# Kernel tuning notes

Hardware: AMD Instinct MI355X
Metric: run time of the kernel (lower is better)

## Reference

```python
import jax, jax.numpy as jnp
import numpy as np


def _mlp(x, w1, b1, w2, b2):
    # Linear -> Softplus -> Linear, matching nn.Sequential(Linear, Softplus, Linear)
    h = jax.nn.softplus(jnp.dot(x, w1.T) + b1)
    return jnp.dot(h, w2.T) + b2


def _forward(X, SC, w_init1, b_init1, w_init2, b_init2, w_eta1, b_eta1, w_eta2, b_eta2):
    N, L, _ = X.shape
    I = X[..., 1:2]   # [N, L, 1] current
    T = X[..., 2:3]   # [N, L, 1] temperature
    U = X[..., 3:4]   # [N, L, 1] voltage
    R = SC[..., 2:3]  # [N, 1]

    # SOC_init = SC[...,3:4] * (1 + SOC_init_net([I0, T0, U0, R]))
    init_feats = jnp.concatenate([I[:, 0], T[:, 0], U[:, 0], R], axis=-1)  # [N, 4]
    soc_init = SC[..., 3:4] * (1.0 + _mlp(init_feats, w_init1, b_init1, w_init2, b_init2))  # [N, 1]

    # delta_eta = eta_net([I, T])
    delta_eta = _mlp(jnp.concatenate([I, T], axis=-1), w_eta1, b_eta1, w_eta2, b_eta2)  # [N, L, 1]

    X_obs = jnp.concatenate([I, T, U, delta_eta], axis=-1)  # [N, L, 4]

    Q = SC[:, None, 0:1]      # [N, 1, 1]
    eta_0 = SC[:, None, 1:2]  # [N, 1, 1]
    # dy/dt does not depend on y -> Euler loop is an exact prefix sum.
    dy_dt = eta_0 * (1.0 + delta_eta) * I / (3600.0 * Q)  # [N, L, 1]

    # t_mask is all-True, so dt uses all 4 columns of X_obs (as in the source).
    dt = X_obs[:, 1:, :] - X_obs[:, :-1, :]        # [N, L-1, 4]
    inc = dt * dy_dt[:, :-1, :]                    # [N, L-1, 4]
    y_rest = soc_init[:, None, :] + jnp.cumsum(inc, axis=1)          # [N, L-1, 4]
    y0 = jnp.broadcast_to(soc_init[:, None, :], (N, 1, 4))           # [N, 1, 4]
    return jnp.concatenate([y0, y_rest], axis=1)   # [N, L, 4] == stack(dim=0).transpose(0,1)


def setup_inputs() -> dict:
    key = jax.random.key(0)
    ks = jax.random.split(key, 6)
    N, L = 4096, 4096
    X = jax.random.normal(ks[0], (N, L, 4), dtype=jnp.float32)
    # SC = [Q, eta_0, R, SOC_init_scale]; shift away from 0 so Q in denominator is safe
    SC = jax.random.uniform(ks[1], (N, 4), dtype=jnp.float32, minval=0.1, maxval=1.1)
    std = 0.1  # init_network_weights default
    return {
        "X": X,
        "SC": SC,
        "w_init1": std * jax.random.normal(ks[2], (1, 4), dtype=jnp.float32),
        "b_init1": jnp.zeros((1,), dtype=jnp.float32),
        "w_init2": std * jax.random.normal(ks[3], (1, 1), dtype=jnp.float32),
        "b_init2": jnp.zeros((1,), dtype=jnp.float32),
        "w_eta1": std * jax.random.normal(ks[4], (1, 2), dtype=jnp.float32),
        "b_eta1": jnp.zeros((1,), dtype=jnp.float32),
        "w_eta2": std * jax.random.normal(ks[5], (1, 1), dtype=jnp.float32),
        "b_eta2": jnp.zeros((1,), dtype=jnp.float32),
    }


def reference(X, SC, w_init1, b_init1, w_init2, b_init2, w_eta1, b_eta1, w_eta2, b_eta2):
    return _forward(X, SC, w_init1, b_init1, w_init2, b_init2,
                    w_eta1, b_eta1, w_eta2, b_eta2)
```

## Files before the change

### kernel.cpp

```cpp
#include <hip/hip_runtime.h>
#include <math.h>

#define BLOCK 256
#define NW (BLOCK / 64)

typedef float f32x4 __attribute__((ext_vector_type(4)));

__device__ __forceinline__ float sp(float x) {
    return fmaxf(x, 0.0f) + __logf(1.0f + __expf(-fabsf(x)));
}

__device__ __forceinline__ float wave_scan_f32(float s) {
    s += __int_as_float(__builtin_amdgcn_update_dpp(0, __float_as_int(s), 0x111, 0xf, 0xf, false));
    s += __int_as_float(__builtin_amdgcn_update_dpp(0, __float_as_int(s), 0x112, 0xf, 0xf, false));
    s += __int_as_float(__builtin_amdgcn_update_dpp(0, __float_as_int(s), 0x114, 0xf, 0xf, false));
    s += __int_as_float(__builtin_amdgcn_update_dpp(0, __float_as_int(s), 0x118, 0xf, 0xf, false));
    s += __int_as_float(__builtin_amdgcn_update_dpp(0, __float_as_int(s), 0x142, 0xa, 0xf, false));
    s += __int_as_float(__builtin_amdgcn_update_dpp(0, __float_as_int(s), 0x143, 0xc, 0xf, false));
    return s;
}

__device__ __forceinline__ void lds_barrier() {
    asm volatile("s_waitcnt lgkmcnt(0)\n\ts_barrier" ::: "memory");
}

__global__ __launch_bounds__(BLOCK) void socnet_kernel(
    const f32x4* __restrict__ X,
    const float*  __restrict__ SC,
    const float*  __restrict__ wi1, const float* __restrict__ bi1,
    const float*  __restrict__ wi2, const float* __restrict__ bi2,
    const float*  __restrict__ we1, const float* __restrict__ be1,
    const float*  __restrict__ we2, const float* __restrict__ be2,
    f32x4* __restrict__ Y, int L)
{
    const int n    = blockIdx.x;
    const int t    = threadIdx.x;
    const int wid  = t >> 6;

    const size_t rowoff = (size_t)n * (size_t)L;
    const f32x4* Xr = X + rowoff;
    f32x4*       Yr = Y + rowoff;

    const float W10 = we1[0], W11 = we1[1], B1 = be1[0];
    const float W2  = we2[0], B2e = be2[0];

    const float Q    = SC[n * 4 + 0];
    const float eta0 = SC[n * 4 + 1];
    const float R    = SC[n * 4 + 2];
    const float S3   = SC[n * 4 + 3];
    const float inv  = eta0 / (3600.0f * Q);

    const f32x4 x0 = Xr[0];
    const float h0 = sp(wi1[0] * x0.y + wi1[1] * x0.z + wi1[2] * x0.w + wi1[3] * R + bi1[0]);
    const float soc = S3 * (1.0f + (wi2[0] * h0 + bi2[0]));

    __shared__ f32x4 s_wsum[2][NW];

    f32x4 carry = (f32x4)(0.0f);

    const int ntiles = L / BLOCK;
    const int Lm1 = L - 1;

    int p = t;
    f32x4 xc0 = Xr[p];
    f32x4 xn0 = Xr[(p + 1 < L) ? (p + 1) : Lm1];
    f32x4 xc1 = Xr[(p + BLOCK < L) ? (p + BLOCK) : Lm1];
    f32x4 xn1 = Xr[(p + BLOCK + 1 < L) ? (p + BLOCK + 1) : Lm1];

    for (int tile = 0; tile < ntiles; ++tile) {
        const int pc = (p + 2 * BLOCK < L) ? (p + 2 * BLOCK) : Lm1;
        const int pn = (p + 2 * BLOCK + 1 < L) ? (p + 2 * BLOCK + 1) : Lm1;
        const f32x4 xc2 = Xr[pc];
        const f32x4 xn2 = Xr[pn];

        const float de_c = W2 * sp(W10 * xc0.y + W11 * xc0.z + B1) + B2e;
        const float de_n = W2 * sp(W10 * xn0.y + W11 * xn0.z + B1) + B2e;
        const float dy   = inv * (1.0f + de_c) * xc0.y;

        f32x4 inc;
        inc.x = (xn0.y - xc0.y) * dy;
        inc.y = (xn0.z - xc0.z) * dy;
        inc.z = (xn0.w - xc0.w) * dy;
        inc.w = (de_n - de_c) * dy;

        f32x4 scn;
        scn.x = wave_scan_f32(inc.x);
        scn.y = wave_scan_f32(inc.y);
        scn.z = wave_scan_f32(inc.z);
        scn.w = wave_scan_f32(inc.w);

        if ((t & 63) == 63) s_wsum[tile & 1][wid] = scn;
        lds_barrier();

        f32x4 excl = carry + scn - inc;
        #pragma unroll
        for (int w = 0; w < NW; ++w) {
            const f32x4 ws = s_wsum[tile & 1][w];
            if (w < wid) excl += ws;
            carry += ws;
        }

        const f32x4 yv = excl + (f32x4)(soc);
        __builtin_nontemporal_store(yv, &Yr[p]);

        xc0 = xc1; xn0 = xn1;
        xc1 = xc2; xn1 = xn2;
        p += BLOCK;
    }
}

extern "C" void kernel_launch(void* const* d_in, const int* in_sizes, int n_in,
                              void* d_out, int out_size, void* d_ws, size_t ws_size,
                              hipStream_t stream) {
    const f32x4* X   = (const f32x4*)d_in[0];
    const float* SC  = (const float*)d_in[1];
    const float* wi1 = (const float*)d_in[2];
    const float* bi1 = (const float*)d_in[3];
    const float* wi2 = (const float*)d_in[4];
    const float* bi2 = (const float*)d_in[5];
    const float* we1 = (const float*)d_in[6];
    const float* be1 = (const float*)d_in[7];
    const float* we2 = (const float*)d_in[8];
    const float* be2 = (const float*)d_in[9];
    f32x4* Y = (f32x4*)d_out;

    const int N = in_sizes[1] / 4;
    const int L = in_sizes[0] / (4 * N);

    socnet_kernel<<<N, BLOCK, 0, stream>>>(X, SC, wi1, bi1, wi2, bi2,
                                           we1, be1, we2, be2, Y, L);
}
```

Before: 93.54 us.

## Share neighbor observations via LDS instead of reloading shifted X rows

Each thread now loads only its own X element and computes its eta MLP value once, writing both to a double-buffered LDS array so the thread to its left can read them as its 'next' element. This removes the second shifted global load per element and the duplicate softplus evaluation. The prefetch depth goes from two tiles to three. The cost is extra LDS traffic, and the write into the next buffer relies on the existing per-tile barrier for ordering, which adds a dependency between tiles.

```diff
diff --git a/kernel.cpp b/kernel.cpp
--- a/kernel.cpp
+++ b/kernel.cpp
@@ -54,6 +54,7 @@
     const float h0 = sp(wi1[0] * x0.y + wi1[1] * x0.z + wi1[2] * x0.w + wi1[3] * R + bi1[0]);
     const float soc = S3 * (1.0f + (wi2[0] * h0 + bi2[0]));
 
+    __shared__ f32x4 s_obs[2][BLOCK + 1];
     __shared__ f32x4 s_wsum[2][NW];
 
     f32x4 carry = (f32x4)(0.0f);
@@ -63,25 +64,44 @@
 
     int p = t;
     f32x4 xc0 = Xr[p];
-    f32x4 xn0 = Xr[(p + 1 < L) ? (p + 1) : Lm1];
-    f32x4 xc1 = Xr[(p + BLOCK < L) ? (p + BLOCK) : Lm1];
-    f32x4 xn1 = Xr[(p + BLOCK + 1 < L) ? (p + BLOCK + 1) : Lm1];
+    f32x4 xc1 = Xr[(p + BLOCK     <= Lm1) ? p + BLOCK     : Lm1];
+    f32x4 xc2 = Xr[(p + 2 * BLOCK <= Lm1) ? p + 2 * BLOCK : Lm1];
+
+    float de0 = W2 * sp(W10 * xc0.y + W11 * xc0.z + B1) + B2e;
+    {
+        f32x4 ob; ob.x = xc0.y; ob.y = xc0.z; ob.z = xc0.w; ob.w = de0;
+        s_obs[0][t] = ob;
+        if (t == 0) {
+            const float d = W2 * sp(W10 * xc1.y + W11 * xc1.z + B1) + B2e;
+            f32x4 ob2; ob2.x = xc1.y; ob2.y = xc1.z; ob2.z = xc1.w; ob2.w = d;
+            s_obs[0][BLOCK] = ob2;
+        }
+    }
+    lds_barrier();
 
     for (int tile = 0; tile < ntiles; ++tile) {
-        const int pc = (p + 2 * BLOCK < L) ? (p + 2 * BLOCK) : Lm1;
-        const int pn = (p + 2 * BLOCK + 1 < L) ? (p + 2 * BLOCK + 1) : Lm1;
-        const f32x4 xc2 = Xr[pc];
-        const f32x4 xn2 = Xr[pn];
+        int ip = p + 3 * BLOCK; if (ip > Lm1) ip = Lm1;
+        const f32x4 xc3 = Xr[ip];
 
-        const float de_c = W2 * sp(W10 * xc0.y + W11 * xc0.z + B1) + B2e;
-        const float de_n = W2 * sp(W10 * xn0.y + W11 * xn0.z + B1) + B2e;
-        const float dy   = inv * (1.0f + de_c) * xc0.y;
+        const f32x4 nb = s_obs[tile & 1][t + 1];
 
+        const float de1 = W2 * sp(W10 * xc1.y + W11 * xc1.z + B1) + B2e;
+        {
+            f32x4 ob; ob.x = xc1.y; ob.y = xc1.z; ob.z = xc1.w; ob.w = de1;
+            s_obs[(tile + 1) & 1][t] = ob;
+            if (t == 0) {
+                const float d2 = W2 * sp(W10 * xc2.y + W11 * xc2.z + B1) + B2e;
+                f32x4 ob2; ob2.x = xc2.y; ob2.y = xc2.z; ob2.z = xc2.w; ob2.w = d2;
+                s_obs[(tile + 1) & 1][BLOCK] = ob2;
+            }
+        }
+
+        const float dy = inv * (1.0f + de0) * xc0.y;
         f32x4 inc;
-        inc.x = (xn0.y - xc0.y) * dy;
-        inc.y = (xn0.z - xc0.z) * dy;
-        inc.z = (xn0.w - xc0.w) * dy;
-        inc.w = (de_n - de_c) * dy;
+        inc.x = (nb.x - xc0.y) * dy;
+        inc.y = (nb.y - xc0.z) * dy;
+        inc.z = (nb.z - xc0.w) * dy;
+        inc.w = (nb.w - de0)  * dy;
 
         f32x4 scn;
         scn.x = wave_scan_f32(inc.x);
@@ -103,8 +123,9 @@
         const f32x4 yv = excl + (f32x4)(soc);
         __builtin_nontemporal_store(yv, &Yr[p]);
 
-        xc0 = xc1; xn0 = xn1;
-        xc1 = xc2; xn1 = xn2;
+        xc0 = xc1; de0 = de1;
+        xc1 = xc2;
+        xc2 = xc3;
         p += BLOCK;
     }
 }
```

After: 89.19 us, median of 2. 4.7% less time.

## Process two timesteps per thread and share neighbor values through LDS

Applied to the files above, without the earlier changes.

Each thread now handles an even/odd pair of consecutive timesteps, so one block iteration covers twice as many elements. The next-element values are exchanged through a double-buffered LDS array instead of being reloaded from global memory, which removes the duplicate neighbor load and halves the number of scans and barriers per element. Launch bounds now also request higher occupancy. In exchange there is extra LDS traffic, per-thread register pressure and a serial dependency within each pair.

```diff
diff --git a/kernel.cpp b/kernel.cpp
--- a/kernel.cpp
+++ b/kernel.cpp
@@ -3,6 +3,7 @@
 
 #define BLOCK 256
 #define NW (BLOCK / 64)
+#define TILE (BLOCK * 2)
 
 typedef float f32x4 __attribute__((ext_vector_type(4)));
 
@@ -24,7 +25,7 @@
     asm volatile("s_waitcnt lgkmcnt(0)\n\ts_barrier" ::: "memory");
 }
 
-__global__ __launch_bounds__(BLOCK) void socnet_kernel(
+__global__ __launch_bounds__(BLOCK, 8) void socnet_kernel(
     const f32x4* __restrict__ X,
     const float*  __restrict__ SC,
     const float*  __restrict__ wi1, const float* __restrict__ bi1,
@@ -54,58 +55,96 @@
     const float h0 = sp(wi1[0] * x0.y + wi1[1] * x0.z + wi1[2] * x0.w + wi1[3] * R + bi1[0]);
     const float soc = S3 * (1.0f + (wi2[0] * h0 + bi2[0]));
 
+    __shared__ f32x4 s_obsE[2][BLOCK + 1];
     __shared__ f32x4 s_wsum[2][NW];
 
     f32x4 carry = (f32x4)(0.0f);
 
-    const int ntiles = L / BLOCK;
+    const int ntiles = L / TILE;
     const int Lm1 = L - 1;
 
-    int p = t;
-    f32x4 xc0 = Xr[p];
-    f32x4 xn0 = Xr[(p + 1 < L) ? (p + 1) : Lm1];
-    f32x4 xc1 = Xr[(p + BLOCK < L) ? (p + BLOCK) : Lm1];
-    f32x4 xn1 = Xr[(p + BLOCK + 1 < L) ? (p + BLOCK + 1) : Lm1];
+    const int pe = 2 * t;
+    f32x4 xE0 = Xr[pe];
+    f32x4 xO0 = Xr[pe + 1];
+    int i1e = pe + TILE;     if (i1e > Lm1) i1e = Lm1;
+    int i1o = pe + TILE + 1; if (i1o > Lm1) i1o = Lm1;
+    f32x4 xE1 = Xr[i1e];
+    f32x4 xO1 = Xr[i1o];
 
-    for (int tile = 0; tile < ntiles; ++tile) {
-        const int pc = (p + 2 * BLOCK < L) ? (p + 2 * BLOCK) : Lm1;
-        const int pn = (p + 2 * BLOCK + 1 < L) ? (p + 2 * BLOCK + 1) : Lm1;
-        const f32x4 xc2 = Xr[pc];
-        const f32x4 xn2 = Xr[pn];
+    float deE0 = W2 * sp(W10 * xE0.y + W11 * xE0.z + B1) + B2e;
 
-        const float de_c = W2 * sp(W10 * xc0.y + W11 * xc0.z + B1) + B2e;
-        const float de_n = W2 * sp(W10 * xn0.y + W11 * xn0.z + B1) + B2e;
-        const float dy   = inv * (1.0f + de_c) * xc0.y;
+    {
+        f32x4 ob; ob.x = xE0.y; ob.y = xE0.z; ob.z = xE0.w; ob.w = deE0;
+        s_obsE[0][t] = ob;
+        if (t == 0) {
+            const float d = W2 * sp(W10 * xE1.y + W11 * xE1.z + B1) + B2e;
+            f32x4 ob2; ob2.x = xE1.y; ob2.y = xE1.z; ob2.z = xE1.w; ob2.w = d;
+            s_obsE[0][BLOCK] = ob2;
+        }
+    }
+    lds_barrier();
 
-        f32x4 inc;
-        inc.x = (xn0.y - xc0.y) * dy;
-        inc.y = (xn0.z - xc0.z) * dy;
-        inc.z = (xn0.w - xc0.w) * dy;
-        inc.w = (de_n - de_c) * dy;
+    for (int j = 0; j < ntiles; ++j) {
+        int i2e = (j + 2) * TILE + pe;     if (i2e > Lm1) i2e = Lm1;
+        int i2o = i2e + 1;                 if (i2o > Lm1) i2o = Lm1;
+        const f32x4 xE2 = Xr[i2e];
+        const f32x4 xO2 = Xr[i2o];
 
+        const f32x4 nb = s_obsE[j & 1][t + 1];
+
+        const float deE1 = W2 * sp(W10 * xE1.y + W11 * xE1.z + B1) + B2e;
+        {
+            f32x4 ob; ob.x = xE1.y; ob.y = xE1.z; ob.z = xE1.w; ob.w = deE1;
+            s_obsE[(j + 1) & 1][t] = ob;
+            if (t == 0) {
+                const float d2 = W2 * sp(W10 * xE2.y + W11 * xE2.z + B1) + B2e;
+                f32x4 ob2; ob2.x = xE2.y; ob2.y = xE2.z; ob2.z = xE2.w; ob2.w = d2;
+                s_obsE[(j + 1) & 1][BLOCK] = ob2;
+            }
+        }
+
+        const float deO0 = W2 * sp(W10 * xO0.y + W11 * xO0.z + B1) + B2e;
+
+        const float dyE = inv * (1.0f + deE0) * xE0.y;
+        f32x4 incE;
+        incE.x = (xO0.y - xE0.y) * dyE;
+        incE.y = (xO0.z - xE0.z) * dyE;
+        incE.z = (xO0.w - xE0.w) * dyE;
+        incE.w = (deO0  - deE0)  * dyE;
+
+        const float dyO = inv * (1.0f + deO0) * xO0.y;
+        f32x4 incO;
+        incO.x = (nb.x - xO0.y) * dyO;
+        incO.y = (nb.y - xO0.z) * dyO;
+        incO.z = (nb.z - xO0.w) * dyO;
+        incO.w = (nb.w - deO0)  * dyO;
+
+        const f32x4 pair = incE + incO;
         f32x4 scn;
-        scn.x = wave_scan_f32(inc.x);
-        scn.y = wave_scan_f32(inc.y);
-        scn.z = wave_scan_f32(inc.z);
-        scn.w = wave_scan_f32(inc.w);
+        scn.x = wave_scan_f32(pair.x);
+        scn.y = wave_scan_f32(pair.y);
+        scn.z = wave_scan_f32(pair.z);
+        scn.w = wave_scan_f32(pair.w);
 
-        if ((t & 63) == 63) s_wsum[tile & 1][wid] = scn;
+        if ((t & 63) == 63) s_wsum[j & 1][wid] = scn;
         lds_barrier();
 
-        f32x4 excl = carry + scn - inc;
+        f32x4 excl = carry + scn - pair;
         #pragma unroll
         for (int w = 0; w < NW; ++w) {
-            const f32x4 ws = s_wsum[tile & 1][w];
+            const f32x4 ws = s_wsum[j & 1][w];
             if (w < wid) excl += ws;
             carry += ws;
         }
 
-        const f32x4 yv = excl + (f32x4)(soc);
-        __builtin_nontemporal_store(yv, &Yr[p]);
+        const f32x4 yE = excl + (f32x4)(soc);
+        const f32x4 yO = yE + incE;
+        f32x4* dst = &Yr[(size_t)j * TILE + pe];
+        __builtin_nontemporal_store(yE, dst);
+        __builtin_nontemporal_store(yO, dst + 1);
 
-        xc0 = xc1; xn0 = xn1;
-        xc1 = xc2; xn1 = xn2;
-        p += BLOCK;
+        xE0 = xE1; xO0 = xO1; deE0 = deE1;
+        xE1 = xE2; xO1 = xO2;
     }
 }
 
```

After: 110.9 us. 18.5% more time.
